# Performance work log

Hardware: AMD Instinct MI355X
Metric: run time of the kernel (lower is better)

## Reference

```python
import jax, jax.numpy as jnp
import numpy as np

S, N, F, H, O = 64, 4096, 32, 64, 2  # seq_len, n_nodes, nfeat, nhid, nout


def setup_inputs() -> dict:
    key = jax.random.key(0)
    ks = jax.random.split(key, 8)
    sc = 0.02
    return {
        "x": jax.random.normal(ks[0], (S, N, F), jnp.float32),
        "adj": jax.random.uniform(ks[1], (N, N), jnp.float32) / N,  # dense normalized-ish adjacency
        "W1": jax.random.normal(ks[2], (F, H), jnp.float32) * sc,
        "b1": jnp.zeros((H,), jnp.float32),
        "W2": jax.random.normal(ks[3], (H, O), jnp.float32) * sc,
        "b2": jnp.zeros((O,), jnp.float32),
        "Wih0": jax.random.normal(ks[4], (3 * H, O * N), jnp.float32) * sc,
        "Whh0": jax.random.normal(ks[5], (3 * H, H), jnp.float32) * sc,
        "bih0": jnp.zeros((3 * H,), jnp.float32),
        "bhh0": jnp.zeros((3 * H,), jnp.float32),
        "Wih1": jax.random.normal(ks[6], (3 * H, H), jnp.float32) * sc,
        "Whh1": jax.random.normal(ks[7], (3 * H, H), jnp.float32) * sc,
        "bih1": jnp.zeros((3 * H,), jnp.float32),
        "bhh1": jnp.zeros((3 * H,), jnp.float32),
    }


def _gru_layer(xs, Wih, Whh, bih, bhh):
    # xs: (S, B, in); PyTorch GRU cell semantics, h0 = 0
    B = xs.shape[1]
    h0 = jnp.zeros((B, Whh.shape[1]), xs.dtype)

    def step(h, x_t):
        gi = x_t @ Wih.T + bih            # (B, 3H)
        gh = h @ Whh.T + bhh              # (B, 3H)
        ir, iz, inn = jnp.split(gi, 3, axis=-1)
        hr, hz, hn = jnp.split(gh, 3, axis=-1)
        r = jax.nn.sigmoid(ir + hr)
        z = jax.nn.sigmoid(iz + hz)
        n = jnp.tanh(inn + r * hn)
        h_new = (1.0 - z) * n + z * h
        return h_new, h_new

    hT, ys = jax.lax.scan(step, h0, xs)
    return ys, hT


def reference(x, adj, W1, b1, W2, b2, Wih0, Whh0, bih0, bhh0, Wih1, Whh1, bih1, bhh1):
    # GCN per timestep (vectorized over time): adj @ (x @ W) + b, relu, adj @ (. @ W2) + b2, log_softmax
    # dropout inactive (eval mode)
    support = jnp.einsum('snf,fh->snh', x, W1) + b1          # (S, N, H)
    h = jnp.einsum('ij,sjh->sih', adj, support)              # (S, N, H)
    h = jax.nn.relu(h)
    support2 = jnp.einsum('snh,ho->sno', h, W2) + b2         # (S, N, O)
    g = jnp.einsum('ij,sjo->sio', adj, support2)             # (S, N, O)
    logp = jax.nn.log_softmax(g, axis=-1)                    # dim=1 of (N, O) per node
    rnn_in = logp.reshape(S, 1, N * O)                       # batch = 1 (torch.stack construction)
    ys0, h0T = _gru_layer(rnn_in, Wih0, Whh0, bih0, bhh0)
    ys1, h1T = _gru_layer(ys0, Wih1, Whh1, bih1, bhh1)
    hn = jnp.stack([h0T, h1T])                               # (n_layers, 1, H)
    return ys1, hn
```

## Files before the change

### kernel.cpp

```cpp
#include <hip/hip_runtime.h>
#include <stdint.h>

#define SS 64
#define NN 4096
#define FF 32
#define HH 64
#define OO 2
#define G3 192

typedef float f32x4 __attribute__((ext_vector_type(4)));
typedef short bf16x8 __attribute__((ext_vector_type(8)));
typedef unsigned short u16x8 __attribute__((ext_vector_type(8)));
typedef long longx2 __attribute__((ext_vector_type(2)));

#define AS1 __attribute__((address_space(1)))
#define AS3 __attribute__((address_space(3)))

__device__ __forceinline__ unsigned short f2bf(float f) {
  union { float f; uint32_t u; } v; v.f = f;
  uint32_t u = v.u;
  uint32_t r = (u + 0x7FFFu + ((u >> 16) & 1u)) >> 16;
  return (unsigned short)r;
}
__device__ __forceinline__ float bf2f(unsigned short s) {
  union { uint32_t u; float f; } v; v.u = ((uint32_t)s) << 16;
  return v.f;
}
__device__ __forceinline__ unsigned char f2e4m3(float x) {
  float a = fabsf(x);
  unsigned s = (x < 0.f) ? 0x80u : 0u;
  if (a >= 448.f) return (unsigned char)(s | 0x7E);
  if (a < 0.015625f) {
    int q = (int)rintf(a * 512.f);
    return (unsigned char)(s | (unsigned)q);
  }
  union { float f; uint32_t u; } v; v.f = a;
  uint32_t b = v.u + 0x7FFFFu + ((v.u >> 20) & 1u);
  int e = (int)(b >> 23) - 127;
  if (e > 8) return (unsigned char)(s | 0x7E);
  return (unsigned char)(s | (unsigned)(((e + 7) << 3) | ((b >> 20) & 7u)));
}
__device__ __forceinline__ int kperm128(int i) {
  int b = (i >> 3) & 15;
  int np = ((b & 7) << 1) | (b >> 3);
  return (i & ~127) | (np << 3) | (i & 7);
}

__global__ __launch_bounds__(256) void k_prep(const float* __restrict__ adj,
                                              unsigned char* __restrict__ adj8,
                                              float* __restrict__ rowsum,
                                              const float* __restrict__ x,
                                              unsigned char* __restrict__ Xt8) {
  __shared__ float xl[64][33];
  __shared__ float ps[4];
  int tid = threadIdx.x;
  if (blockIdx.x < 4096) {
    int row = blockIdx.x;
    const float4* src = (const float4*)(adj + (size_t)row * 4096);
    uchar4* dst8 = (uchar4*)(adj8 + (size_t)row * 4096);
    float sum = 0.f;
    #pragma unroll
    for (int q = 0; q < 4; ++q) {
      int idx = q * 256 + tid;
      float4 v = src[idx];
      uchar4 r8;
      r8.x = f2e4m3(v.x * 4096.f); r8.y = f2e4m3(v.y * 4096.f);
      r8.z = f2e4m3(v.z * 4096.f); r8.w = f2e4m3(v.w * 4096.f);
      int b = (idx >> 1) & 15;
      int np = ((b & 7) << 1) | (b >> 3);
      int nidx = (idx & ~31) | (np << 1) | (idx & 1);
      dst8[nidx] = r8;
      sum += (v.x + v.y) + (v.z + v.w);
    }
    #pragma unroll
    for (int off = 1; off < 64; off <<= 1) sum += __shfl_xor(sum, off);
    if ((tid & 63) == 0) ps[tid >> 6] = sum;
    __syncthreads();
    if (tid == 0) rowsum[row] = (ps[0] + ps[1]) + (ps[2] + ps[3]);
    return;
  }
  int bs = blockIdx.x - 4096;
  int s = bs >> 6, jb = (bs & 63) << 6;
  const float4* xg = (const float4*)(x + ((size_t)s * NN + jb) * FF);
  #pragma unroll
  for (int ii = 0; ii < 2; ++ii) {
    int idx = tid + ii * 256;
    float4 v = xg[idx];
    int j = idx >> 3, f = (idx & 7) << 2;
    xl[j][f] = v.x; xl[j][f + 1] = v.y; xl[j][f + 2] = v.z; xl[j][f + 3] = v.w;
  }
  __syncthreads();
  int f = tid >> 3, jc = tid & 7;
  unsigned int lo = 0, hi = 0;
  #pragma unroll
  for (int jj = 0; jj < 4; ++jj) lo |= ((unsigned int)f2e4m3(xl[jc * 8 + jj][f])) << (jj * 8);
  #pragma unroll
  for (int jj = 0; jj < 4; ++jj) hi |= ((unsigned int)f2e4m3(xl[jc * 8 + 4 + jj][f])) << (jj * 8);
  uint2 ov; ov.x = lo; ov.y = hi;
  int np = (jc << 1) | ((jb >> 6) & 1);
  *(uint2*)(Xt8 + (size_t)(s * 32 + f) * 4096 + (jb & ~127) + np * 8) = ov;
}

#define SBAR()   asm volatile("s_barrier" ::: "memory")
#define VMC8()   asm volatile("s_waitcnt vmcnt(8)" ::: "memory")
#define VMC6()   asm volatile("s_waitcnt vmcnt(6)" ::: "memory")
#define VMC0()   asm volatile("s_waitcnt vmcnt(0)" ::: "memory")

__global__ __launch_bounds__(512, 2) void k_gemmAX(
    const unsigned char* __restrict__ A8,
    const unsigned char* __restrict__ B8,
    const float* __restrict__ rowsum,
    const float* __restrict__ W1f,
    const float* __restrict__ b1f,
    const float* __restrict__ W2f,
    const float* __restrict__ b2f,
    unsigned char* __restrict__ B2t8) {
  __shared__ __align__(16) char lds[147456];
  __shared__ __align__(16) unsigned short w1t[64 * 40];
  __shared__ float w2l[128];
  __shared__ float b1l[64];
  __shared__ float b2l[2];
  const int tid = threadIdx.x;
  const int wid = tid >> 6, l = tid & 63;
  const int wr2 = wid >> 2, wc2 = wid & 3;
  const int lc = l & 15, lq = l >> 4;

  {
    float4 v = ((const float4*)W1f)[tid];
    int f = tid >> 4, h = (tid & 15) * 4;
    w1t[(h + 0) * 40 + f] = f2bf(v.x);
    w1t[(h + 1) * 40 + f] = f2bf(v.y);
    w1t[(h + 2) * 40 + f] = f2bf(v.z);
    w1t[(h + 3) * 40 + f] = f2bf(v.w);
  }
  if (tid < 32) *(float4*)&w2l[tid * 4] = ((const float4*)W2f)[tid];
  if (tid < 16) *(float4*)&b1l[tid * 4] = ((const float4*)b1f)[tid];
  if (tid < 2) b2l[tid] = b2f[tid];
  __syncthreads();

  int bid = blockIdx.x;
  int swz = (bid & 7) * 32 + (bid >> 3);
  const int i0 = (swz >> 3) * 128;
  const int c0 = (swz & 7) * 256;

  const int aBase = (wr2 * 64 + lc) * 128;
  const int bBase = 16384 + (wc2 * 64 + lc) * 128;
  const int cLo = ((lq ^ (lc & 7)) << 4);
  const int cHi = (((4 + lq) ^ (lc & 7)) << 4);

  const int srow = wid * 8 + (l >> 3);
  const int scol = (((l & 7) ^ (srow & 7)) << 4);
  const char* gA = (const char*)A8 + (size_t)(i0 + srow) * 4096 + scol;
  const char* gB = (const char*)B8 + (size_t)(c0 + srow) * 4096 + scol;
  char* ldsW = (char*)lds + wid * 1024;
  const char* ldsR = (const char*)lds;

  f32x4 acc[4][4];
  #pragma unroll
  for (int m = 0; m < 4; ++m)
    #pragma unroll
    for (int n = 0; n < 4; ++n) acc[m][n] = {0.f, 0.f, 0.f, 0.f};

  longx2 afqL[4], bfqL[4], afqH[4], bfqH[4];

#define STAGE6(KT, BOFS) do {                                                        \
    __builtin_amdgcn_global_load_lds((const AS1 void*)(gA + (KT) * 128),             \
        (AS3 void*)(ldsW + (BOFS)), 16, 0, 0);                                       \
    __builtin_amdgcn_global_load_lds((const AS1 void*)(gA + 262144 + (KT) * 128),    \
        (AS3 void*)(ldsW + (BOFS) + 8192), 16, 0, 0);                                \
    __builtin_amdgcn_global_load_lds((const AS1 void*)(gB + (KT) * 128),             \
        (AS3 void*)(ldsW + (BOFS) + 16384), 16, 0, 0);                               \
    __builtin_amdgcn_global_load_lds((const AS1 void*)(gB + 262144 + (KT) * 128),    \
        (AS3 void*)(ldsW + (BOFS) + 24576), 16, 0, 0);                               \
    __builtin_amdgcn_global_load_lds((const AS1 void*)(gB + 524288 + (KT) * 128),    \
        (AS3 void*)(ldsW + (BOFS) + 32768), 16, 0, 0);                               \
    __builtin_amdgcn_global_load_lds((const AS1 void*)(gB + 786432 + (KT) * 128),    \
        (AS3 void*)(ldsW + (BOFS) + 40960), 16, 0, 0);                               \
  } while (0)

#define READ_ALL(BOFS) do {                                                          \
    _Pragma("unroll")                                                                \
    for (int _m = 0; _m < 4; ++_m) {                                                 \
      afqL[_m] = *(const longx2*)(ldsR + (BOFS) + aBase + _m * 2048 + cLo);          \
      afqH[_m] = *(const longx2*)(ldsR + (BOFS) + aBase + _m * 2048 + cHi);          \
    }                                                                                \
    _Pragma("unroll")                                                                \
    for (int _n = 0; _n < 4; ++_n) {                                                 \
      bfqL[_n] = *(const longx2*)(ldsR + (BOFS) + bBase + _n * 2048 + cLo);          \
      bfqH[_n] = *(const longx2*)(ldsR + (BOFS) + bBase + _n * 2048 + cHi);          \
    } } while (0)

#define MFMA_SET(AF, BF) do {                                                        \
    __builtin_amdgcn_s_setprio(1);                                                   \
    _Pragma("unroll")                                                                \
    for (int _kk = 0; _kk < 2; ++_kk)                                                \
      _Pragma("unroll")                                                              \
      for (int _m = 0; _m < 4; ++_m)                                                 \
        _Pragma("unroll")                                                            \
        for (int _n = 0; _n < 4; ++_n)                                               \
          acc[_m][_n] = __builtin_amdgcn_mfma_f32_16x16x32_fp8_fp8(                  \
              AF[_m][_kk], BF[_n][_kk], acc[_m][_n], 0, 0, 0);                       \
    __builtin_amdgcn_s_setprio(0);                                                   \
  } while (0)

  STAGE6(0, 0);
  STAGE6(1, 49152);
  VMC6();
  SBAR();

  int bR = 0, bS = 98304;
  for (int kt = 0; kt < 30; ++kt) {
    READ_ALL(bR);
    STAGE6(kt + 2, bS);
    MFMA_SET(afqL, bfqL);
    MFMA_SET(afqH, bfqH);
    VMC6();
    SBAR();
    bR = (bR == 98304) ? 0 : bR + 49152;
    bS = (bS == 98304) ? 0 : bS + 49152;
  }
  READ_ALL(bR); MFMA_SET(afqL, bfqL); MFMA_SET(afqH, bfqH);
  VMC0(); SBAR(); bR = (bR == 98304) ? 0 : bR + 49152;
  READ_ALL(bR); MFMA_SET(afqL, bfqL); MFMA_SET(afqH, bfqH);
  __syncthreads();

  unsigned short* C1L = (unsigned short*)lds;
  {
    const int rb = wr2 * 64 + lq * 4;
    const int cbL = wc2 * 64 + lc;
    #pragma unroll
    for (int m = 0; m < 4; ++m)
      #pragma unroll
      for (int r = 0; r < 4; ++r) {
        const int row = rb + m * 16 + r;
        #pragma unroll
        for (int n = 0; n < 4; ++n)
          C1L[row * 264 + cbL + n * 16] = f2bf(acc[m][n][r] * 0.000244140625f);
      }
  }
  __syncthreads();

  {
    const f32x4 zacc = {0.f, 0.f, 0.f, 0.f};
    bf16x8 bw[4];
    float b1v[4], w2a[4], w2b[4];
    #pragma unroll
    for (int n = 0; n < 4; ++n) {
      const int h = n * 16 + lc;
      bw[n] = *(const bf16x8*)((const char*)w1t + h * 80 + lq * 16);
      b1v[n] = b1l[h];
      w2a[n] = w2l[h * 2];
      w2b[n] = w2l[h * 2 + 1];
    }
    const int rbase = wid * 16 + lq * 4;
    const float4 rs4 = *(const float4*)&rowsum[i0 + rbase];
    const float bo0 = b2l[0], bo1 = b2l[1];
    #pragma unroll
    for (int s = 0; s < 8; ++s) {
      bf16x8 afe = *(const bf16x8*)((const char*)C1L +
                     (wid * 16 + lc) * 528 + s * 64 + lq * 16);
      float o0r[4] = {0.f, 0.f, 0.f, 0.f};
      float o1r[4] = {0.f, 0.f, 0.f, 0.f};
      #pragma unroll
      for (int n = 0; n < 4; ++n) {
        f32x4 hq = __builtin_amdgcn_mfma_f32_16x16x32_bf16(afe, bw[n], zacc, 0, 0, 0);
        #pragma unroll
        for (int r = 0; r < 4; ++r) {
          float hv = hq[r] + rs4[r] * b1v[n];
          hv = hv > 0.f ? hv : 0.f;
          o0r[r] += hv * w2a[n];
          o1r[r] += hv * w2b[n];
        }
      }
      #pragma unroll
      for (int off = 1; off < 16; off <<= 1)
        #pragma unroll
        for (int r = 0; r < 4; ++r) {
          o0r[r] += __shfl_xor(o0r[r], off);
          o1r[r] += __shfl_xor(o1r[r], off);
        }
      if (lc == 0) {
        const int sg = (c0 >> 5) + s;
        #pragma unroll
        for (int r = 0; r < 4; ++r) {
          const int ip = kperm128(i0 + rbase + r);
          B2t8[(size_t)(sg * 2 + 0) * 4096 + ip] = f2e4m3((o0r[r] + bo0) * 4096.f);
          B2t8[(size_t)(sg * 2 + 1) * 4096 + ip] = f2e4m3((o1r[r] + bo1) * 4096.f);
        }
      }
    }
  }
}

__global__ __launch_bounds__(256) void k_gemm2f8(
    const unsigned char* __restrict__ A8,
    const unsigned char* __restrict__ B8,
    float* __restrict__ Gp) {
  __shared__ __align__(16) char lds[98304];
  const int tid = threadIdx.x;
  const int wid = tid >> 6, l = tid & 63;
  const int wr = wid >> 1, wc = wid & 1;
  const int lc = l & 15, lq = l >> 4;
  const int bi = blockIdx.x & 31, ks = blockIdx.x >> 5;
  const int i0 = bi * 128;
  const size_t kbase = (size_t)ks * 512;

  const int aBase = (wr * 64 + lc) * 128;
  const int bBase = 16384 + (wc * 64 + lc) * 128;
  const int cLo = ((lq ^ (lc & 7)) << 4);
  const int cHi = (((4 + lq) ^ (lc & 7)) << 4);

  const int srow = wid * 8 + (l >> 3);
  const int scol = (((l & 7) ^ (srow & 7)) << 4);
  const char* gA = (const char*)A8 + (size_t)(i0 + srow) * 4096 + kbase + scol;
  const char* gB = (const char*)B8 + (size_t)srow * 4096 + kbase + scol;
  char* ldsW = (char*)lds + wid * 1024;
  const char* ldsR = (const char*)lds;

  f32x4 acc[4][4];
  #pragma unroll
  for (int m = 0; m < 4; ++m)
    #pragma unroll
    for (int n = 0; n < 4; ++n) acc[m][n] = {0.f, 0.f, 0.f, 0.f};

  longx2 afqL[4], bfqL[4], afqH[4], bfqH[4];

#define G2STAGE(KT, BOFS) do {                                                       \
    __builtin_amdgcn_global_load_lds((const AS1 void*)(gA + (KT) * 128),             \
        (AS3 void*)(ldsW + (BOFS)), 16, 0, 0);                                       \
    __builtin_amdgcn_global_load_lds((const AS1 void*)(gA + 131072 + (KT) * 128),    \
        (AS3 void*)(ldsW + (BOFS) + 4096), 16, 0, 0);                                \
    __builtin_amdgcn_global_load_lds((const AS1 void*)(gA + 262144 + (KT) * 128),    \
        (AS3 void*)(ldsW + (BOFS) + 8192), 16, 0, 0);                                \
    __builtin_amdgcn_global_load_lds((const AS1 void*)(gA + 393216 + (KT) * 128),    \
        (AS3 void*)(ldsW + (BOFS) + 12288), 16, 0, 0);                               \
    __builtin_amdgcn_global_load_lds((const AS1 void*)(gB + (KT) * 128),             \
        (AS3 void*)(ldsW + (BOFS) + 16384), 16, 0, 0);                               \
    __builtin_amdgcn_global_load_lds((const AS1 void*)(gB + 131072 + (KT) * 128),    \
        (AS3 void*)(ldsW + (BOFS) + 20480), 16, 0, 0);                               \
    __builtin_amdgcn_global_load_lds((const AS1 void*)(gB + 262144 + (KT) * 128),    \
        (AS3 void*)(ldsW + (BOFS) + 24576), 16, 0, 0);                               \
    __builtin_amdgcn_global_load_lds((const AS1 void*)(gB + 393216 + (KT) * 128),    \
        (AS3 void*)(ldsW + (BOFS) + 28672), 16, 0, 0);                               \
  } while (0)

#define G2READALL(BOFS) do {                                                         \
    _Pragma("unroll")                                                                \
    for (int _m = 0; _m < 4; ++_m) {                                                 \
      afqL[_m] = *(const longx2*)(ldsR + (BOFS) + aBase + _m * 2048 + cLo);          \
      afqH[_m] = *(const longx2*)(ldsR + (BOFS) + aBase + _m * 2048 + cHi);          \
    }                                                                                \
    _Pragma("unroll")                                                                \
    for (int _n = 0; _n < 4; ++_n) {                                                 \
      bfqL[_n] = *(const longx2*)(ldsR + (BOFS) + bBase + _n * 2048 + cLo);          \
      bfqH[_n] = *(const longx2*)(ldsR + (BOFS) + bBase + _n * 2048 + cHi);          \
    } } while (0)

#define G2MFMA(AF, BF) do {                                                          \
    __builtin_amdgcn_s_setprio(1);                                                   \
    _Pragma("unroll")                                                                \
    for (int _kk = 0; _kk < 2; ++_kk)                                                \
      _Pragma("unroll")                                                              \
      for (int _m = 0; _m < 4; ++_m)                                                 \
        _Pragma("unroll")                                                            \
        for (int _n = 0; _n < 4; ++_n)                                               \
          acc[_m][_n] = __builtin_amdgcn_mfma_f32_16x16x32_fp8_fp8(                  \
              AF[_m][_kk], BF[_n][_kk], acc[_m][_n], 0, 0, 0);                       \
    __builtin_amdgcn_s_setprio(0);                                                   \
  } while (0)

  G2STAGE(0, 0);
  G2STAGE(1, 32768);
  VMC8();
  SBAR();

  G2READALL(0); G2STAGE(2, 65536); G2MFMA(afqL, bfqL); G2MFMA(afqH, bfqH);
  VMC8(); SBAR();
  G2READALL(32768); G2STAGE(3, 0); G2MFMA(afqL, bfqL); G2MFMA(afqH, bfqH);
  VMC8(); SBAR();
  G2READALL(65536); G2MFMA(afqL, bfqL); G2MFMA(afqH, bfqH);
  VMC0(); SBAR();
  G2READALL(0); G2MFMA(afqL, bfqL); G2MFMA(afqH, bfqH);

  float* outp = Gp + (size_t)ks * 524288;
  const int rbase = i0 + wr * 64 + lq * 4;
  const int cbase = wc * 64 + lc;
  #pragma unroll
  for (int m = 0; m < 4; ++m)
    #pragma unroll
    for (int n = 0; n < 4; ++n)
      #pragma unroll
      for (int r = 0; r < 4; ++r)
        outp[(size_t)(rbase + m * 16 + r) * 128 + cbase + n * 16] =
            acc[m][n][r] * 5.9604644775390625e-8f;
}

__global__ __launch_bounds__(256) void k_lsm(const float* __restrict__ Gp,
                                             float* __restrict__ Rm) {
  __shared__ float Gacc[32][130];
  int i0 = blockIdx.x * 32;
  int tid = threadIdx.x;
  float4 v[4];
  #pragma unroll
  for (int i = 0; i < 4; ++i) v[i] = {0.f, 0.f, 0.f, 0.f};
  for (int ks = 0; ks < 8; ++ks) {
    const float4* gp4 = ((const float4*)Gp) + (size_t)ks * 131072 + (size_t)i0 * 32;
    #pragma unroll
    for (int i = 0; i < 4; ++i) {
      float4 t = gp4[tid + i * 256];
      v[i].x += t.x; v[i].y += t.y; v[i].z += t.z; v[i].w += t.w;
    }
  }
  #pragma unroll
  for (int i = 0; i < 4; ++i) {
    int f4i = tid + i * 256, row = f4i >> 5, c = (f4i & 31) * 4;
    Gacc[row][c] = v[i].x; Gacc[row][c + 1] = v[i].y;
    Gacc[row][c + 2] = v[i].z; Gacc[row][c + 3] = v[i].w;
  }
  __syncthreads();
  #pragma unroll
  for (int j = 0; j < 8; ++j) {
    int p = j * 256 + tid;
    int ii = p & 31, s = p >> 5;
    float g0 = Gacc[ii][s * 2], g1 = Gacc[ii][s * 2 + 1];
    float m = fmaxf(g0, g1);
    float lse = m + logf(expf(g0 - m) + expf(g1 - m));
    float2 o_; o_.x = g0 - lse; o_.y = g1 - lse;
    *((float2*)(Rm + (size_t)s * 8192 + (size_t)(i0 + ii) * 2)) = o_;
  }
}

__global__ __launch_bounds__(256) void k_gi0(const float* __restrict__ Rm,
                                             const float* __restrict__ Wih0,
                                             float* __restrict__ part) {
  __shared__ float4 Wl[4 * 128];
  int gb = blockIdx.x % 48, ks = blockIdx.x / 48;
  int c0 = ks * 512;
  int tid = threadIdx.x;
  #pragma unroll
  for (int i = 0; i < 2; ++i) {
    int idx = tid + i * 256;
    int g = idx >> 7, c4 = idx & 127;
    Wl[g * 128 + c4] = ((const float4*)(Wih0 + (size_t)(gb * 4 + g) * 8192 + c0))[c4];
  }
  __syncthreads();
  int w = tid >> 6, lane = tid & 63;
  for (int pass = 0; pass < 16; ++pass) {
    int t = pass * 4 + w;
    float a0 = 0.f, a1 = 0.f, a2 = 0.f, a3 = 0.f;
    const float4* rg = (const float4*)(Rm + (size_t)t * 8192 + c0);
    #pragma unroll
    for (int i = 0; i < 2; ++i) {
      int c4 = i * 64 + lane;
      float4 r4 = rg[c4];
      float4 w0 = Wl[c4], w1 = Wl[128 + c4], w2 = Wl[256 + c4], w3 = Wl[384 + c4];
      a0 += r4.x * w0.x + r4.y * w0.y + r4.z * w0.z + r4.w * w0.w;
      a1 += r4.x * w1.x + r4.y * w1.y + r4.z * w1.z + r4.w * w1.w;
      a2 += r4.x * w2.x + r4.y * w2.y + r4.z * w2.z + r4.w * w2.w;
      a3 += r4.x * w3.x + r4.y * w3.y + r4.z * w3.z + r4.w * w3.w;
    }
    #pragma unroll
    for (int off = 1; off < 64; off <<= 1) {
      a0 += __shfl_xor(a0, off);
      a1 += __shfl_xor(a1, off);
      a2 += __shfl_xor(a2, off);
      a3 += __shfl_xor(a3, off);
    }
    if (lane == 0) {
      float4 o_; o_.x = a0; o_.y = a1; o_.z = a2; o_.w = a3;
      *((float4*)(part + ((size_t)ks * 64 + t) * 192 + gb * 4)) = o_;
    }
  }
}

__global__ __launch_bounds__(256) void k_gi0red(const float* __restrict__ part,
                                                const float* __restrict__ bih0,
                                                float* __restrict__ gi0) {
  int idx = blockIdx.x * 256 + threadIdx.x;
  if (idx < 12288) {
    float s_ = bih0[idx % 192];
    for (int ks = 0; ks < 16; ++ks) s_ += part[ks * 12288 + idx];
    gi0[idx] = s_;
  }
}

__device__ __forceinline__ float fsigm(float x) {
  return __builtin_amdgcn_rcpf(1.f + __expf(-x));
}
__device__ __forceinline__ float ftanh(float x) {
  return 1.f - 2.f * __builtin_amdgcn_rcpf(1.f + __expf(2.f * x));
}

__global__ __launch_bounds__(384) void k_gru(const float* __restrict__ gi0,
                                             const float* __restrict__ Whh0,
                                             const float* __restrict__ bhh0,
                                             const float* __restrict__ Wih1,
                                             const float* __restrict__ Whh1,
                                             const float* __restrict__ bih1,
                                             const float* __restrict__ bhh1,
                                             float* __restrict__ out) {
  __shared__ float gil[64][192];
  __shared__ float gout[576];
  __shared__ __align__(16) unsigned short hv[2][64];
  const int tid = threadIdx.x;
  const int w = tid >> 6, l = tid & 63;
  const int matw = w >> 1, half = w & 1;
  const float* Wm = (matw == 0) ? Whh0 : (matw == 1 ? Wih1 : Whh1);
  const int mi = (matw == 2) ? 1 : 0;

  bf16x8 afr[6][2];
  #pragma unroll
  for (int rbi = 0; rbi < 6; ++rbi) {
    int g = (half * 6 + rbi) * 16 + (l & 15);
    #pragma unroll
    for (int kh = 0; kh < 2; ++kh) {
      int k0 = kh * 32 + (l >> 4) * 8;
      const float4* src = (const float4*)(Wm + (size_t)g * 64 + k0);
      float4 v0 = src[0], v1 = src[1];
      bf16x8 a;
      a[0] = (short)f2bf(v0.x); a[1] = (short)f2bf(v0.y);
      a[2] = (short)f2bf(v0.z); a[3] = (short)f2bf(v0.w);
      a[4] = (short)f2bf(v1.x); a[5] = (short)f2bf(v1.y);
      a[6] = (short)f2bf(v1.z); a[7] = (short)f2bf(v1.w);
      afr[rbi][kh] = a;
    }
  }
  {
    float4* gf = (float4*)&gil[0][0];
    const float4* gs = (const float4*)gi0;
    #pragma unroll
    for (int i = 0; i < 8; ++i) gf[i * 384 + tid] = gs[i * 384 + tid];
  }
  if (tid < 128) hv[tid >> 6][tid & 63] = 0;

  float hreg = 0.f;
  float bR = 0.f, bZ = 0.f, bNa = 0.f, bNb = 0.f;
  if (tid < 64) {
    bR = bhh0[tid]; bZ = bhh0[64 + tid]; bNa = bhh0[128 + tid];
  } else if (tid < 128) {
    int g = tid - 64;
    bR = bih1[g] + bhh1[g];
    bZ = bih1[64 + g] + bhh1[64 + g];
    bNa = bih1[128 + g];
    bNb = bhh1[128 + g];
  }
  asm volatile("s_waitcnt lgkmcnt(0)\n\ts_barrier" ::: "memory");

  const int gwb = matw * 192 + half * 96 + (l >> 4) * 4;
  const f32x4 zacc = {0.f, 0.f, 0.f, 0.f};

  for (int i = 0; i <= 64; ++i) {
    bf16x8 b0 = *(const bf16x8*)&hv[mi][(l >> 4) * 8];
    bf16x8 b1 = *(const bf16x8*)&hv[mi][32 + (l >> 4) * 8];
    #pragma unroll
    for (int rbi = 0; rbi < 6; ++rbi) {
      f32x4 a_ = __builtin_amdgcn_mfma_f32_16x16x32_bf16(afr[rbi][0], b0, zacc, 0, 0, 0);
      a_ = __builtin_amdgcn_mfma_f32_16x16x32_bf16(afr[rbi][1], b1, a_, 0, 0, 0);
      if (!(l & 15)) *(f32x4*)&gout[gwb + rbi * 16] = a_;
    }
    asm volatile("s_waitcnt lgkmcnt(0)\n\ts_barrier" ::: "memory");
    if (tid < 64) {
      if (i < 64) {
        float r = fsigm(gil[i][tid] + gout[tid] + bR);
        float z = fsigm(gil[i][64 + tid] + gout[64 + tid] + bZ);
        float n = ftanh(gil[i][128 + tid] + r * (gout[128 + tid] + bNa));
        hreg = (1.f - z) * n + z * hreg;
        hv[0][tid] = f2bf(hreg);
      }
    } else if (tid < 128 && i > 0) {
      int g = tid - 64;
      float r = fsigm(gout[192 + g] + gout[384 + g] + bR);
      float z = fsigm(gout[256 + g] + gout[448 + g] + bZ);
      float n = ftanh((gout[320 + g] + bNa) + r * (gout[512 + g] + bNb));
      hreg = (1.f - z) * n + z * hreg;
      hv[1][g] = f2bf(hreg);
      out[(i - 1) * 64 + g] = hreg;
    }
    asm volatile("s_waitcnt lgkmcnt(0)\n\ts_barrier" ::: "memory");
  }
  if (tid < 64) out[4096 + tid] = hreg;
  else if (tid < 128) out[4096 + 64 + (tid - 64)] = hreg;
}

extern "C" void kernel_launch(void* const* d_in, const int* in_sizes, int n_in,
                              void* d_out, int out_size, void* d_ws, size_t ws_size,
                              hipStream_t stream) {
  const float* x    = (const float*)d_in[0];
  const float* adj  = (const float*)d_in[1];
  const float* W1   = (const float*)d_in[2];
  const float* b1   = (const float*)d_in[3];
  const float* W2   = (const float*)d_in[4];
  const float* b2   = (const float*)d_in[5];
  const float* Wih0 = (const float*)d_in[6];
  const float* Whh0 = (const float*)d_in[7];
  const float* bih0 = (const float*)d_in[8];
  const float* bhh0 = (const float*)d_in[9];
  const float* Wih1 = (const float*)d_in[10];
  const float* Whh1 = (const float*)d_in[11];
  const float* bih1 = (const float*)d_in[12];
  const float* bhh1 = (const float*)d_in[13];
  float* out = (float*)d_out;

  char* ws = (char*)d_ws;
  unsigned char* adj8  = (unsigned char*)ws;
  unsigned char* Xt8   = (unsigned char*)(ws + 16777216);
  float* rowsum        = (float*)(ws + 25165824);
  float* Gp            = (float*)(ws + 25182208);
  float* Rm            = (float*)(ws + 41959424);
  float* part          = (float*)(ws + 44056576);
  float* gi0           = (float*)(ws + 44843008);
  unsigned char* B2t8  = (unsigned char*)(ws + 44892160);

  k_prep<<<8192, 256, 0, stream>>>(adj, adj8, rowsum, x, Xt8);
  k_gemmAX<<<256, 512, 0, stream>>>(adj8, Xt8, rowsum, W1, b1, W2, b2, B2t8);
  k_gemm2f8<<<256, 256, 0, stream>>>(adj8, B2t8, Gp);
  k_lsm<<<128, 256, 0, stream>>>(Gp, Rm);
  k_gi0<<<768, 256, 0, stream>>>(Rm, Wih0, part);
  k_gi0red<<<48, 256, 0, stream>>>(part, bih0, gi0);
  k_gru<<<1, 384, 0, stream>>>(gi0, Whh0, bhh0, Wih1, Whh1, bih1, bhh1, out);
}
```

Measured before the change: 148.4 us.

## Halve split-K in fp8 adjacency GEMM and shrink GRU kernel to three waves

The second adjacency GEMM now covers twice the K range per block (1024 instead of 512), so it launches 128 blocks instead of 256. Its K loop becomes a rolled 6-iteration pipeline over a triple LDS buffer, and the log-softmax reduction sums 4 partial slices instead of 8. Separately, the single-block GRU recurrence drops from 6 to 3 waves, with each wave computing all 12 row blocks of one weight matrix. The intent is to cut partial-sum traffic and reduction work, and to shorten barrier cost in the serial GRU. In exchange, 128 blocks leave part of the MI355X's compute units idle during the GEMM, and each GRU wave does twice as many MFMAs per step on a serial critical path.

```diff
diff --git a/kernel.cpp b/kernel.cpp
--- a/kernel.cpp
+++ b/kernel.cpp
@@ -303,7 +303,7 @@
   const int lc = l & 15, lq = l >> 4;
   const int bi = blockIdx.x & 31, ks = blockIdx.x >> 5;
   const int i0 = bi * 128;
-  const size_t kbase = (size_t)ks * 512;
+  const size_t kbase = (size_t)ks * 1024;
 
   const int aBase = (wr * 64 + lc) * 128;
   const int bBase = 16384 + (wc * 64 + lc) * 128;
@@ -374,13 +374,20 @@
   VMC8();
   SBAR();
 
-  G2READALL(0); G2STAGE(2, 65536); G2MFMA(afqL, bfqL); G2MFMA(afqH, bfqH);
-  VMC8(); SBAR();
-  G2READALL(32768); G2STAGE(3, 0); G2MFMA(afqL, bfqL); G2MFMA(afqH, bfqH);
-  VMC8(); SBAR();
-  G2READALL(65536); G2MFMA(afqL, bfqL); G2MFMA(afqH, bfqH);
-  VMC0(); SBAR();
-  G2READALL(0); G2MFMA(afqL, bfqL); G2MFMA(afqH, bfqH);
+  int bR = 0, bS = 65536;
+  for (int kt = 0; kt < 6; ++kt) {
+    G2READALL(bR);
+    G2STAGE(kt + 2, bS);
+    G2MFMA(afqL, bfqL);
+    G2MFMA(afqH, bfqH);
+    VMC8();
+    SBAR();
+    bR = (bR == 65536) ? 0 : bR + 32768;
+    bS = (bS == 65536) ? 0 : bS + 32768;
+  }
+  G2READALL(bR); G2MFMA(afqL, bfqL); G2MFMA(afqH, bfqH);
+  VMC0(); SBAR(); bR = (bR == 65536) ? 0 : bR + 32768;
+  G2READALL(bR); G2MFMA(afqL, bfqL); G2MFMA(afqH, bfqH);
 
   float* outp = Gp + (size_t)ks * 524288;
   const int rbase = i0 + wr * 64 + lq * 4;
@@ -403,7 +410,7 @@
   float4 v[4];
   #pragma unroll
   for (int i = 0; i < 4; ++i) v[i] = {0.f, 0.f, 0.f, 0.f};
-  for (int ks = 0; ks < 8; ++ks) {
+  for (int ks = 0; ks < 4; ++ks) {
     const float4* gp4 = ((const float4*)Gp) + (size_t)ks * 131072 + (size_t)i0 * 32;
     #pragma unroll
     for (int i = 0; i < 4; ++i) {
@@ -491,30 +498,31 @@
   return 1.f - 2.f * __builtin_amdgcn_rcpf(1.f + __expf(2.f * x));
 }
 
-__global__ __launch_bounds__(384) void k_gru(const float* __restrict__ gi0,
-                                             const float* __restrict__ Whh0,
-                                             const float* __restrict__ bhh0,
-                                             const float* __restrict__ Wih1,
-                                             const float* __restrict__ Whh1,
-                                             const float* __restrict__ bih1,
-                                             const float* __restrict__ bhh1,
-                                             float* __restrict__ out) {
+__global__ __launch_bounds__(192, 1) void k_gru(const float* __restrict__ gi0,
+                                                const float* __restrict__ Whh0,
+                                                const float* __restrict__ bhh0,
+                                                const float* __restrict__ Wih1,
+                                                const float* __restrict__ Whh1,
+                                                const float* __restrict__ bih1,
+                                                const float* __restrict__ bhh1,
+                                                float* __restrict__ out) {
   __shared__ float gil[64][192];
   __shared__ float gout[576];
   __shared__ __align__(16) unsigned short hv[2][64];
   const int tid = threadIdx.x;
   const int w = tid >> 6, l = tid & 63;
-  const int matw = w >> 1, half = w & 1;
+  const int matw = w;
   const float* Wm = (matw == 0) ? Whh0 : (matw == 1 ? Wih1 : Whh1);
   const int mi = (matw == 2) ? 1 : 0;
-
-  bf16x8 afr[6][2];
-  #pragma unroll
-  for (int rbi = 0; rbi < 6; ++rbi) {
-    int g = (half * 6 + rbi) * 16 + (l & 15);
+  const int lc = l & 15, lq = l >> 4;
+
+  bf16x8 afr[12][2];
+  #pragma unroll
+  for (int rbi = 0; rbi < 12; ++rbi) {
+    int g = rbi * 16 + lc;
     #pragma unroll
     for (int kh = 0; kh < 2; ++kh) {
-      int k0 = kh * 32 + (l >> 4) * 8;
+      int k0 = kh * 32 + lq * 8;
       const float4* src = (const float4*)(Wm + (size_t)g * 64 + k0);
       float4 v0 = src[0], v1 = src[1];
       bf16x8 a;
@@ -529,7 +537,7 @@
     float4* gf = (float4*)&gil[0][0];
     const float4* gs = (const float4*)gi0;
     #pragma unroll
-    for (int i = 0; i < 8; ++i) gf[i * 384 + tid] = gs[i * 384 + tid];
+    for (int i = 0; i < 16; ++i) gf[i * 192 + tid] = gs[i * 192 + tid];
   }
   if (tid < 128) hv[tid >> 6][tid & 63] = 0;
 
@@ -546,17 +554,17 @@
   }
   asm volatile("s_waitcnt lgkmcnt(0)\n\ts_barrier" ::: "memory");
 
-  const int gwb = matw * 192 + half * 96 + (l >> 4) * 4;
+  const int gwb = matw * 192 + lq * 4;
   const f32x4 zacc = {0.f, 0.f, 0.f, 0.f};
 
   for (int i = 0; i <= 64; ++i) {
-    bf16x8 b0 = *(const bf16x8*)&hv[mi][(l >> 4) * 8];
-    bf16x8 b1 = *(const bf16x8*)&hv[mi][32 + (l >> 4) * 8];
-    #pragma unroll
-    for (int rbi = 0; rbi < 6; ++rbi) {
+    bf16x8 b0 = *(const bf16x8*)&hv[mi][lq * 8];
+    bf16x8 b1 = *(const bf16x8*)&hv[mi][32 + lq * 8];
+    #pragma unroll
+    for (int rbi = 0; rbi < 12; ++rbi) {
       f32x4 a_ = __builtin_amdgcn_mfma_f32_16x16x32_bf16(afr[rbi][0], b0, zacc, 0, 0, 0);
       a_ = __builtin_amdgcn_mfma_f32_16x16x32_bf16(afr[rbi][1], b1, a_, 0, 0, 0);
-      if (!(l & 15)) *(f32x4*)&gout[gwb + rbi * 16] = a_;
+      if (lc == 0) *(f32x4*)&gout[gwb + rbi * 16] = a_;
     }
     asm volatile("s_waitcnt lgkmcnt(0)\n\ts_barrier" ::: "memory");
     if (tid < 64) {
@@ -613,9 +621,9 @@
 
   k_prep<<<8192, 256, 0, stream>>>(adj, adj8, rowsum, x, Xt8);
   k_gemmAX<<<256, 512, 0, stream>>>(adj8, Xt8, rowsum, W1, b1, W2, b2, B2t8);
-  k_gemm2f8<<<256, 256, 0, stream>>>(adj8, B2t8, Gp);
+  k_gemm2f8<<<128, 256, 0, stream>>>(adj8, B2t8, Gp);
   k_lsm<<<128, 256, 0, stream>>>(Gp, Rm);
   k_gi0<<<768, 256, 0, stream>>>(Rm, Wih0, part);
   k_gi0red<<<48, 256, 0, stream>>>(part, bih0, gi0);
-  k_gru<<<1, 384, 0, stream>>>(gi0, Whh0, bhh0, Wih1, Whh1, bih1, bhh1, out);
-}
+  k_gru<<<1, 192, 0, stream>>>(gi0, Whh0, bhh0, Wih1, Whh1, bih1, bhh1, out);
+}
```

After: 158.9 us. 7.1% more time.
